# Optimization experiments

Hardware: AMD Instinct MI355X
Metric: run time of the kernel (lower is better)

The kernel has to match this reference:

```python
import jax, jax.numpy as jnp
import numpy as np

ALPHA = 0.2  # LeakyReLU negative slope
EPS = 1e-8


def setup_inputs() -> dict:
    key = jax.random.key(0)
    ks = jax.random.split(key, 7)
    N, Fin, Fout, E = 100000, 256, 128, 800000
    node_embedding = jax.random.normal(ks[0], (N, Fin), dtype=jnp.float32)
    adj_pos = jax.random.randint(ks[1], (2, E), 0, N, dtype=jnp.int64)
    adj_neg = jax.random.randint(ks[2], (2, E), 0, N, dtype=jnp.int64)
    edge_embedding = jax.random.normal(ks[3], (2, Fout), dtype=jnp.float32)
    Wr = jax.random.normal(ks[4], (2, Fin, Fout), dtype=jnp.float32) * 0.05
    a = jax.random.normal(ks[5], (1, 2 * Fout), dtype=jnp.float32) * 0.05
    bias = jax.random.normal(ks[6], (1, Fout), dtype=jnp.float32) * 0.05
    return dict(node_embedding=node_embedding, edge_embedding=edge_embedding,
                Wr=Wr, a=a, bias=bias, adj_pos=adj_pos, adj_neg=adj_neg)


def reference(node_embedding, edge_embedding, Wr, a, bias, adj_pos, adj_neg):
    N = node_embedding.shape[0]
    Fout = Wr.shape[2]
    # h_r = X @ Wr[r], then column-scale by edge_embedding[r] (== mm with diag)
    h_pos = (node_embedding @ Wr[0]) * edge_embedding[0]  # [N, Fout]
    h_neg = (node_embedding @ Wr[1]) * edge_embedding[1]  # [N, Fout]
    a_src = a[0, :Fout]  # attention weights for source half of concat
    a_dst = a[0, Fout:]  # attention weights for dest half

    def edge_scores(h, adj):
        # a . [h[src], h[dst]] computed as node-level dots then scalar gather
        s = h @ a_src  # [N]
        d = h @ a_dst  # [N]
        z = s[adj[0]] + d[adj[1]]  # [E]
        z = jnp.where(z > 0, z, ALPHA * z)  # LeakyReLU
        return jax.nn.sigmoid(z)

    e_pos = edge_scores(h_pos, adj_pos)  # [E_pos]
    e_neg = edge_scores(h_neg, adj_neg)  # [E_neg]

    # row-sum normalizer: spmm(edge, edge_e, ones) == segment_sum over row idx
    rows = jnp.concatenate([adj_pos[0], adj_neg[0]])
    e_all = jnp.concatenate([e_pos, e_neg])
    row_sum = jax.ops.segment_sum(e_all, rows, num_segments=N) + EPS  # [N]

    # weighted aggregation: out[i] = sum_{(i,j)} e_ij * h[j]
    agg = (jax.ops.segment_sum(e_pos[:, None] * h_pos[adj_pos[1]], adj_pos[0], num_segments=N)
           + jax.ops.segment_sum(e_neg[:, None] * h_neg[adj_neg[1]], adj_neg[0], num_segments=N))
    return agg / row_sum[:, None] + bias
```

## Files before the change

kernel.cpp:

```cpp
#include <hip/hip_runtime.h>

#define ALPHA 0.2f
#define EPSV 1e-8f
#define BUCK_BITS 8
#define BUCK (1 << BUCK_BITS)
#define CAP 5120
#define EPB_A 4096
#define EPT_A (EPB_A / 256)

typedef float f32x4 __attribute__((ext_vector_type(4)));
typedef short bf16x8 __attribute__((ext_vector_type(8)));

static __device__ __forceinline__ unsigned short f2bf(float f) {
    union { float f; unsigned int u; } c; c.f = f;
    unsigned int u = c.u;
    unsigned int round = ((u >> 16) & 1) + 0x7FFF;
    return (unsigned short)((u + round) >> 16);
}
static __device__ __forceinline__ float bflo(unsigned int u) {
    union { unsigned int u; float f; } c; c.u = u << 16; return c.f;
}
static __device__ __forceinline__ float bfhi(unsigned int u) {
    union { unsigned int u; float f; } c; c.u = u & 0xFFFF0000u; return c.f;
}

__global__ __launch_bounds__(256) void convB_kernel(
    const float* __restrict__ Wr, uint4* __restrict__ Bp)
{
    const int t = blockIdx.x * blockDim.x + threadIdx.x;
    if (t >= 32 * 256) return;
    const int kb  = t >> 8;
    const int col = t & 255;
    const int rel = col >> 7;
    const int cc  = col & 127;
    unsigned short v[8];
    #pragma unroll
    for (int jj = 0; jj < 8; ++jj) {
        const int k = kb * 8 + jj;
        v[jj] = f2bf(Wr[(size_t)rel * 256 * 128 + (size_t)k * 128 + cc]);
    }
    Bp[t] = *reinterpret_cast<const uint4*>(v);
}

__global__ __launch_bounds__(256) void gemm_binA_kernel(
    const float* __restrict__ X, const uint4* __restrict__ Bp,
    const float* __restrict__ ee, const float* __restrict__ a,
    unsigned int* __restrict__ h32, float* __restrict__ sd,
    const int* __restrict__ adj_pos, const int* __restrict__ adj_neg,
    int* __restrict__ bucketCount, unsigned int* __restrict__ edges_tmp,
    int N, int E, int binBlocks)
{
    __shared__ char smem[16384];
    const int tid = threadIdx.x;

    if ((int)blockIdx.x < binBlocks) {
        int* hist = (int*)smem;
        int* base = hist + 512;
        int* cur  = base + 512;
        const int bb = blockIdx.x;
        const long long e0 = (long long)bb * EPB_A;
        const long long twoE = 2LL * E;

        hist[tid] = 0;
        hist[tid + 256] = 0;

        int esrc[EPT_A];
        unsigned int erec[EPT_A];
        #pragma unroll
        for (int k = 0; k < EPT_A; ++k) {
            const long long idx = e0 + (long long)k * 256 + tid;
            if (idx < twoE) {
                const int rel = (idx >= E) ? 1 : 0;
                const long long eidx = rel ? idx - E : idx;
                const int* __restrict__ adj = rel ? adj_neg : adj_pos;
                const int src = adj[eidx];
                const int dst = adj[E + eidx];
                esrc[k] = src;
                erec[k] = (unsigned int)dst | ((unsigned int)rel << 17) |
                          ((unsigned int)(src & (BUCK - 1)) << 18);
            } else {
                esrc[k] = -1;
            }
        }
        __syncthreads();

        #pragma unroll
        for (int k = 0; k < EPT_A; ++k)
            if (esrc[k] >= 0) atomicAdd(&hist[esrc[k] >> BUCK_BITS], 1);
        __syncthreads();

        {
            const int rot = (bb * 61) & 511;
            #pragma unroll
            for (int q = 0; q < 2; ++q) {
                const int t2 = (tid + q * 256 + rot) & 511;
                const int hv = hist[t2];
                base[t2] = hv ? atomicAdd(&bucketCount[t2], hv) : 0;
                cur[t2] = 0;
            }
        }
        __syncthreads();

        #pragma unroll
        for (int k = 0; k < EPT_A; ++k) {
            if (esrc[k] >= 0) {
                const int b = esrc[k] >> BUCK_BITS;
                const int r = atomicAdd(&cur[b], 1);
                const int pos = base[b] + r;
                if (pos < CAP)
                    edges_tmp[(size_t)b * CAP + pos] = erec[k];
            }
        }
        return;
    }

    unsigned short* Alds = (unsigned short*)smem;
    const int lane = tid & 63;
    const int w    = tid >> 6;
    const int wm   = w >> 1;
    const int wn   = w & 1;
    const int cl   = lane & 15;
    const int g    = lane >> 4;
    const int gb   = blockIdx.x - binBlocks;
    const int tile0 = gb * 32;

    {
        float4 fa[4], fb[4];
        #pragma unroll
        for (int pass = 0; pass < 4; ++pass) {
            const int L  = pass * 256 + tid;
            const int r  = L >> 5;
            const int c8 = L & 31;
            const int row = tile0 + r;
            fa[pass] = make_float4(0.f, 0.f, 0.f, 0.f);
            fb[pass] = make_float4(0.f, 0.f, 0.f, 0.f);
            if (row < N) {
                const float* xp = &X[(size_t)row * 256 + c8 * 8];
                fa[pass] = *reinterpret_cast<const float4*>(xp);
                fb[pass] = *reinterpret_cast<const float4*>(xp + 4);
            }
        }
        #pragma unroll
        for (int pass = 0; pass < 4; ++pass) {
            const int L  = pass * 256 + tid;
            const int r  = L >> 5;
            const int c8 = L & 31;
            unsigned short v[8];
            v[0]=f2bf(fa[pass].x); v[1]=f2bf(fa[pass].y);
            v[2]=f2bf(fa[pass].z); v[3]=f2bf(fa[pass].w);
            v[4]=f2bf(fb[pass].x); v[5]=f2bf(fb[pass].y);
            v[6]=f2bf(fb[pass].z); v[7]=f2bf(fb[pass].w);
            const int su = c8 ^ (r & 7);
            *reinterpret_cast<bf16x8*>(&Alds[r * 256 + su * 8]) =
                *reinterpret_cast<const bf16x8*>(v);
        }
    }
    __syncthreads();

    f32x4 acc[8];
    #pragma unroll
    for (int ct = 0; ct < 8; ++ct)
        acc[ct] = (f32x4){0.f, 0.f, 0.f, 0.f};

    const int rl = wm * 16 + cl;
    #pragma unroll
    for (int kc = 0; kc < 8; ++kc) {
        const int ku = kc * 4 + g;
        const bf16x8 af = *reinterpret_cast<const bf16x8*>(
            &Alds[rl * 256 + (ku ^ (rl & 7)) * 8]);
        bf16x8 bfr[8];
        #pragma unroll
        for (int ct = 0; ct < 8; ++ct) {
            const int col = wn * 128 + ct * 16 + cl;
            bfr[ct] = *reinterpret_cast<const bf16x8*>(Bp + ku * 256 + col);
        }
        #pragma unroll
        for (int ct = 0; ct < 8; ++ct)
            acc[ct] = __builtin_amdgcn_mfma_f32_16x16x32_bf16(
                af, bfr[ct], acc[ct], 0, 0, 0);
    }

    const int rt = gb * 2 + wm;
    float eev[8], asv[8], adv[8];
    #pragma unroll
    for (int ct = 0; ct < 8; ++ct) {
        const int col = wn * 128 + ct * 16 + cl;
        const int cc  = col & 127;
        eev[ct] = ee[col];
        asv[ct] = a[cc];
        adv[ct] = a[128 + cc];
    }

    float s_acc[4], d_acc[4];
    #pragma unroll
    for (int reg = 0; reg < 4; ++reg) {
        const int row = rt * 16 + g * 4 + reg;
        const bool ok = row < N;
        float sp = 0.f, dp = 0.f;
        float vv[8];
        #pragma unroll
        for (int ct = 0; ct < 8; ++ct) {
            vv[ct] = acc[ct][reg] * eev[ct];
            sp += vv[ct] * asv[ct];
            dp += vv[ct] * adv[ct];
        }
        if (ok) {
            #pragma unroll
            for (int q = 0; q < 4; ++q) {
                const unsigned int u =
                    (unsigned int)f2bf(vv[2 * q]) |
                    ((unsigned int)f2bf(vv[2 * q + 1]) << 16);
                h32[((size_t)wn * N + row) * 64 + q * 16 + cl] = u;
            }
        }
        s_acc[reg] = sp;
        d_acc[reg] = dp;
    }
    #pragma unroll
    for (int reg = 0; reg < 4; ++reg) {
        float sp = s_acc[reg], dp = d_acc[reg];
        #pragma unroll
        for (int off = 1; off < 16; off <<= 1) {
            sp += __shfl_xor(sp, off);
            dp += __shfl_xor(dp, off);
        }
        if (cl == 0) {
            const int row = rt * 16 + g * 4 + reg;
            if (row < N) {
                sd[(size_t)wn * 2 * N + row]     = sp;
                sd[(size_t)wn * 2 * N + N + row] = dp;
            }
        }
    }
}

__global__ __launch_bounds__(512) void sortB_kernel(
    const int* __restrict__ bucketCount, const unsigned int* __restrict__ edges_tmp,
    const float* __restrict__ sd,
    uint2* __restrict__ edges_final,
    int* __restrict__ rowBeg, int* __restrict__ rowEnd,
    float* __restrict__ rowSum, int N)
{
    __shared__ int hist[BUCK];
    __shared__ int cur[BUCK];
    __shared__ int ssum[BUCK];
    __shared__ float sSrc[2][BUCK];
    __shared__ float rsLds[BUCK];
    const int tid = threadIdx.x;
    const int b   = blockIdx.x;
    const int s0  = b << BUCK_BITS;
    const size_t tb = (size_t)b * CAP;
    const int cnt = min(bucketCount[b], CAP);

    if (tid < BUCK) {
        hist[tid] = 0;
        rsLds[tid] = 0.f;
        const int gsrc = s0 + tid;
        sSrc[0][tid] = (gsrc < N) ? sd[gsrc] : 0.f;
        sSrc[1][tid] = (gsrc < N) ? sd[2 * (size_t)N + gsrc] : 0.f;
    }
    __syncthreads();
    for (int j = tid; j < cnt; j += 512)
        atomicAdd(&hist[edges_tmp[tb + j] >> 18], 1);
    __syncthreads();

    int h0 = 0, incl = 0;
    if (tid < BUCK) { h0 = hist[tid]; ssum[tid] = h0; incl = h0; }
    __syncthreads();
    for (int off = 1; off < BUCK; off <<= 1) {
        const int u = (tid < BUCK && tid >= off) ? ssum[tid - off] : 0;
        __syncthreads();
        if (tid < BUCK) { incl += u; ssum[tid] = incl; }
        __syncthreads();
    }
    if (tid < BUCK) {
        const int excl = incl - h0;
        cur[tid] = excl;
        const int gidx = s0 + tid;
        if (gidx < N) {
            rowBeg[gidx] = (int)tb + excl;
            rowEnd[gidx] = (int)tb + incl;
        }
    }
    __syncthreads();
    for (int j = tid; j < cnt; j += 512) {
        const unsigned int r = edges_tmp[tb + j];
        const int sl  = r >> 18;
        const int rel = (r >> 17) & 1;
        const int dst = r & 0x1FFFF;
        float z = sSrc[rel][sl] + sd[(size_t)rel * 2 * N + N + dst];
        z = z > 0.f ? z : ALPHA * z;
        const float ev = 1.f / (1.f + __expf(-z));
        const int pos = atomicAdd(&cur[sl], 1);
        atomicAdd(&rsLds[sl], ev);
        edges_final[tb + pos] =
            make_uint2((unsigned int)(rel * N + dst), __float_as_uint(ev));
    }
    __syncthreads();
    if (tid < BUCK) {
        const int gidx = s0 + tid;
        if (gidx < N) rowSum[gidx] = rsLds[tid];
    }
}

__global__ __launch_bounds__(256) void gather_kernel(
    const int* __restrict__ rowBeg, const int* __restrict__ rowEnd,
    const float* __restrict__ rowSum,
    const uint2* __restrict__ edges,
    const unsigned int* __restrict__ h32,
    const float* __restrict__ bias, float* __restrict__ out, int N)
{
    const long long gw = ((long long)blockIdx.x * blockDim.x + threadIdx.x) >> 6;
    const int lane = threadIdx.x & 63;
    if (gw >= N) return;
    const int n = (int)gw;

    const int beg = rowBeg[n];
    const int end = rowEnd[n];
    const unsigned loff = (unsigned)(lane << 2);
    const char* __restrict__ hb = (const char*)h32;

    float ax = 0.f, ay = 0.f;
    int j = beg;
    for (; j + 8 <= end; j += 8) {
        uint2 r[8];
        #pragma unroll
        for (int k = 0; k < 8; ++k) r[k] = edges[j + k];
        unsigned int hv[8];
        #pragma unroll
        for (int k = 0; k < 8; ++k)
            hv[k] = *reinterpret_cast<const unsigned int*>(
                hb + ((r[k].x << 8) + loff));
        #pragma unroll
        for (int k = 0; k < 8; ++k) {
            const float e = __uint_as_float(r[k].y);
            ax += e * bflo(hv[k]);
            ay += e * bfhi(hv[k]);
        }
    }
    for (; j + 4 <= end; j += 4) {
        uint2 r[4];
        #pragma unroll
        for (int k = 0; k < 4; ++k) r[k] = edges[j + k];
        unsigned int hv[4];
        #pragma unroll
        for (int k = 0; k < 4; ++k)
            hv[k] = *reinterpret_cast<const unsigned int*>(
                hb + ((r[k].x << 8) + loff));
        #pragma unroll
        for (int k = 0; k < 4; ++k) {
            const float e = __uint_as_float(r[k].y);
            ax += e * bflo(hv[k]);
            ay += e * bfhi(hv[k]);
        }
    }
    for (; j < end; ++j) {
        const uint2 r = edges[j];
        const unsigned int hv = *reinterpret_cast<const unsigned int*>(
            hb + ((r.x << 8) + loff));
        const float e = __uint_as_float(r.y);
        ax += e * bflo(hv);
        ay += e * bfhi(hv);
    }
    const float inv = 1.f / (rowSum[n] + EPSV);
    const int q  = lane >> 4;
    const int cl = lane & 15;
    const int c0 = q * 32 + cl;
    const int c1 = c0 + 16;
    out[(size_t)n * 128 + c0] = ax * inv + bias[c0];
    out[(size_t)n * 128 + c1] = ay * inv + bias[c1];
}

extern "C" void kernel_launch(void* const* d_in, const int* in_sizes, int n_in,
                              void* d_out, int out_size, void* d_ws, size_t ws_size,
                              hipStream_t stream) {
    const float* X      = (const float*)d_in[0];
    const float* ee     = (const float*)d_in[1];
    const float* Wr     = (const float*)d_in[2];
    const float* a      = (const float*)d_in[3];
    const float* bias   = (const float*)d_in[4];
    const int* adj_pos  = (const int*)d_in[5];
    const int* adj_neg  = (const int*)d_in[6];

    const int N = in_sizes[0] / 256;
    const int E = in_sizes[5] / 2;
    const int twoE = 2 * E;
    float* out = (float*)d_out;

    const int gemmBlocks = (N + 31) / 32;
    const int NBUCK = (N + BUCK - 1) >> BUCK_BITS;
    const int binBlocks = (twoE + EPB_A - 1) / EPB_A;

    char* ws = (char*)d_ws;
    uint4* Bp = (uint4*)ws;
    char* p = ws + 32 * 256 * 16;
    unsigned int* h32 = (unsigned int*)p; p += (size_t)2 * N * 64 * 4;
    float* sd         = (float*)p;  p += (size_t)4 * N * 4;
    int* bucketCount  = (int*)p;    p += 512 * 4;
    int* rowBeg       = (int*)p;    p += (size_t)N * 4;
    int* rowEnd       = (int*)p;    p += (size_t)N * 4;
    float* rowSum     = (float*)p;  p += (size_t)N * 4;
    p = (char*)(((uintptr_t)p + 15) & ~(uintptr_t)15);
    unsigned int* edges_tmp = (unsigned int*)p; p += (size_t)NBUCK * CAP * 4;
    uint2* edges_final = (uint2*)p; p += (size_t)NBUCK * CAP * 8;

    (void)hipMemsetAsync(bucketCount, 0, 512 * sizeof(int), stream);

    convB_kernel<<<32, 256, 0, stream>>>(Wr, Bp);

    gemm_binA_kernel<<<binBlocks + gemmBlocks, 256, 0, stream>>>(
        X, Bp, ee, a, h32, sd, adj_pos, adj_neg, bucketCount, edges_tmp,
        N, E, binBlocks);

    sortB_kernel<<<NBUCK, 512, 0, stream>>>(
        bucketCount, edges_tmp, sd, edges_final, rowBeg, rowEnd, rowSum, N);

    gather_kernel<<<(int)(((long long)N * 64 + 255) / 256), 256, 0, stream>>>(
        rowBeg, rowEnd, rowSum, edges_final, h32, bias, out, N);
}
```

Before: 161.4 us.

## Pack edge weight as 14-bit fixed point into index word and interleave bin/gemm blocks

Edge records in the sorted list shrink from 8 bytes (index plus float weight) to one 32-bit word: an 18-bit node index with a 14-bit quantized sigmoid weight. The gather kernel reads four or eight records with vector loads after an alignment prologue. This halves edge-list traffic in the sort and gather stages. In exchange the attention weights lose precision, and the row sum stays in full precision, so normalization is slightly inconsistent. Separately, binning blocks are spread evenly among GEMM blocks in launch order rather than all launched first, to balance memory-bound and compute-bound work across the device.

```diff
diff --git a/kernel.cpp b/kernel.cpp
--- a/kernel.cpp
+++ b/kernel.cpp
@@ -7,6 +7,7 @@
 #define CAP 5120
 #define EPB_A 4096
 #define EPT_A (EPB_A / 256)
+#define EQ_SCALE 16383.f
 
 typedef float f32x4 __attribute__((ext_vector_type(4)));
 typedef short bf16x8 __attribute__((ext_vector_type(8)));
@@ -48,16 +49,20 @@
     unsigned int* __restrict__ h32, float* __restrict__ sd,
     const int* __restrict__ adj_pos, const int* __restrict__ adj_neg,
     int* __restrict__ bucketCount, unsigned int* __restrict__ edges_tmp,
-    int N, int E, int binBlocks)
+    int N, int E, int binBlocks, int totalBlocks)
 {
     __shared__ char smem[16384];
     const int tid = threadIdx.x;
 
-    if ((int)blockIdx.x < binBlocks) {
+    const long long bi = blockIdx.x;
+    const int fi  = (int)((bi * (long long)binBlocks) / totalBlocks);
+    const int fi1 = (int)(((bi + 1) * (long long)binBlocks) / totalBlocks);
+
+    if (fi1 > fi) {
         int* hist = (int*)smem;
         int* base = hist + 512;
         int* cur  = base + 512;
-        const int bb = blockIdx.x;
+        const int bb = fi;
         const long long e0 = (long long)bb * EPB_A;
         const long long twoE = 2LL * E;
 
@@ -121,7 +126,7 @@
     const int wn   = w & 1;
     const int cl   = lane & 15;
     const int g    = lane >> 4;
-    const int gb   = blockIdx.x - binBlocks;
+    const int gb   = (int)bi - fi;
     const int tile0 = gb * 32;
 
     {
@@ -237,7 +242,7 @@
 __global__ __launch_bounds__(512) void sortB_kernel(
     const int* __restrict__ bucketCount, const unsigned int* __restrict__ edges_tmp,
     const float* __restrict__ sd,
-    uint2* __restrict__ edges_final,
+    unsigned int* __restrict__ edges_final,
     int* __restrict__ rowBeg, int* __restrict__ rowEnd,
     float* __restrict__ rowSum, int N)
 {
@@ -293,8 +298,8 @@
         const float ev = 1.f / (1.f + __expf(-z));
         const int pos = atomicAdd(&cur[sl], 1);
         atomicAdd(&rsLds[sl], ev);
-        edges_final[tb + pos] =
-            make_uint2((unsigned int)(rel * N + dst), __float_as_uint(ev));
+        const unsigned int q = (unsigned int)(ev * EQ_SCALE + 0.5f);
+        edges_final[tb + pos] = (q << 18) | (unsigned int)(rel * N + dst);
     }
     __syncthreads();
     if (tid < BUCK) {
@@ -306,7 +311,7 @@
 __global__ __launch_bounds__(256) void gather_kernel(
     const int* __restrict__ rowBeg, const int* __restrict__ rowEnd,
     const float* __restrict__ rowSum,
-    const uint2* __restrict__ edges,
+    const unsigned int* __restrict__ edges,
     const unsigned int* __restrict__ h32,
     const float* __restrict__ bias, float* __restrict__ out, int N)
 {
@@ -319,46 +324,56 @@
     const int end = rowEnd[n];
     const unsigned loff = (unsigned)(lane << 2);
     const char* __restrict__ hb = (const char*)h32;
+    const float esc = 1.f / EQ_SCALE;
 
     float ax = 0.f, ay = 0.f;
     int j = beg;
+
+    for (; j < end && (j & 3); ++j) {
+        const unsigned int r = edges[j];
+        const unsigned int hv = *reinterpret_cast<const unsigned int*>(
+            hb + (((r & 0x3FFFFu) << 8) + loff));
+        const float e = (float)(r >> 18) * esc;
+        ax += e * bflo(hv);
+        ay += e * bfhi(hv);
+    }
     for (; j + 8 <= end; j += 8) {
-        uint2 r[8];
-        #pragma unroll
-        for (int k = 0; k < 8; ++k) r[k] = edges[j + k];
+        const uint4 qa = *reinterpret_cast<const uint4*>(&edges[j]);
+        const uint4 qb = *reinterpret_cast<const uint4*>(&edges[j + 4]);
+        const unsigned int rr[8] = {qa.x, qa.y, qa.z, qa.w,
+                                    qb.x, qb.y, qb.z, qb.w};
         unsigned int hv[8];
         #pragma unroll
         for (int k = 0; k < 8; ++k)
             hv[k] = *reinterpret_cast<const unsigned int*>(
-                hb + ((r[k].x << 8) + loff));
+                hb + (((rr[k] & 0x3FFFFu) << 8) + loff));
         #pragma unroll
         for (int k = 0; k < 8; ++k) {
-            const float e = __uint_as_float(r[k].y);
+            const float e = (float)(rr[k] >> 18) * esc;
             ax += e * bflo(hv[k]);
             ay += e * bfhi(hv[k]);
         }
     }
     for (; j + 4 <= end; j += 4) {
-        uint2 r[4];
-        #pragma unroll
-        for (int k = 0; k < 4; ++k) r[k] = edges[j + k];
+        const uint4 qa = *reinterpret_cast<const uint4*>(&edges[j]);
+        const unsigned int rr[4] = {qa.x, qa.y, qa.z, qa.w};
         unsigned int hv[4];
         #pragma unroll
         for (int k = 0; k < 4; ++k)
             hv[k] = *reinterpret_cast<const unsigned int*>(
-                hb + ((r[k].x << 8) + loff));
+                hb + (((rr[k] & 0x3FFFFu) << 8) + loff));
         #pragma unroll
         for (int k = 0; k < 4; ++k) {
-            const float e = __uint_as_float(r[k].y);
+            const float e = (float)(rr[k] >> 18) * esc;
             ax += e * bflo(hv[k]);
             ay += e * bfhi(hv[k]);
         }
     }
     for (; j < end; ++j) {
-        const uint2 r = edges[j];
+        const unsigned int r = edges[j];
         const unsigned int hv = *reinterpret_cast<const unsigned int*>(
-            hb + ((r.x << 8) + loff));
-        const float e = __uint_as_float(r.y);
+            hb + (((r & 0x3FFFFu) << 8) + loff));
+        const float e = (float)(r >> 18) * esc;
         ax += e * bflo(hv);
         ay += e * bfhi(hv);
     }
@@ -390,6 +405,7 @@
     const int gemmBlocks = (N + 31) / 32;
     const int NBUCK = (N + BUCK - 1) >> BUCK_BITS;
     const int binBlocks = (twoE + EPB_A - 1) / EPB_A;
+    const int totalBlocks = binBlocks + gemmBlocks;
 
     char* ws = (char*)d_ws;
     uint4* Bp = (uint4*)ws;
@@ -402,15 +418,16 @@
     float* rowSum     = (float*)p;  p += (size_t)N * 4;
     p = (char*)(((uintptr_t)p + 15) & ~(uintptr_t)15);
     unsigned int* edges_tmp = (unsigned int*)p; p += (size_t)NBUCK * CAP * 4;
-    uint2* edges_final = (uint2*)p; p += (size_t)NBUCK * CAP * 8;
+    p = (char*)(((uintptr_t)p + 15) & ~(uintptr_t)15);
+    unsigned int* edges_final = (unsigned int*)p; p += (size_t)NBUCK * CAP * 4;
 
     (void)hipMemsetAsync(bucketCount, 0, 512 * sizeof(int), stream);
 
     convB_kernel<<<32, 256, 0, stream>>>(Wr, Bp);
 
-    gemm_binA_kernel<<<binBlocks + gemmBlocks, 256, 0, stream>>>(
+    gemm_binA_kernel<<<totalBlocks, 256, 0, stream>>>(
         X, Bp, ee, a, h32, sd, adj_pos, adj_neg, bucketCount, edges_tmp,
-        N, E, binBlocks);
+        N, E, binBlocks, totalBlocks);
 
     sortB_kernel<<<NBUCK, 512, 0, stream>>>(
         bucketCount, edges_tmp, sd, edges_final, rowBeg, rowEnd, rowSum, N);
```

New measurement: 157.8 us. 2.2% less time.
